# Optimization experiments

Measured on AMD Instinct MI355X. Metric: run time of the kernel, lower is better.

The kernel has to match this reference:

```python
import jax, jax.numpy as jnp
import numpy as np

USER_NUM = 100000
ITEM_NUM = 50000
N_NODES = USER_NUM + ITEM_NUM
EMB = 64
N_LAYERS = 3
E_HALF = 2000000  # edges per direction; total directed edges = 4M


def _make_bipartite_edges(ku, ki):
    u = jax.random.randint(ku, (E_HALF,), 0, USER_NUM)
    i = jax.random.randint(ki, (E_HALF,), 0, ITEM_NUM) + USER_NUM
    # bidirectional: user->item and item->user
    return jnp.concatenate([u, i]), jnp.concatenate([i, u])


def setup_inputs() -> dict:
    key = jax.random.key(0)
    ks = jax.random.split(key, 6)
    U = jax.random.normal(ks[0], (USER_NUM, EMB), jnp.float32)
    I = jax.random.normal(ks[1], (ITEM_NUM, EMB), jnp.float32)
    pos_src, pos_dst = _make_bipartite_edges(ks[2], ks[3])
    neg_src, neg_dst = _make_bipartite_edges(ks[4], ks[5])
    return {"U": U, "I": I, "pos_src": pos_src, "pos_dst": pos_dst,
            "neg_src": neg_src, "neg_dst": neg_dst}


def gcn_layer(x, src, dst):
    # symmetric-normalized sum aggregation (LightGCN propagation)
    ones = jnp.ones(src.shape, x.dtype)
    deg_out = jnp.maximum(jax.ops.segment_sum(ones, src, num_segments=N_NODES), 1.0)
    deg_in = jnp.maximum(jax.ops.segment_sum(ones, dst, num_segments=N_NODES), 1.0)
    h = x * (deg_out ** -0.5)[:, None]          # pre-scale by out-degree
    agg = jax.ops.segment_sum(h[src], dst, num_segments=N_NODES)  # copy_src + sum
    return agg * (deg_in ** -0.5)[:, None]      # post-scale by in-degree


def get_embedding(U, I, src, dst):
    res_u, res_i = U, I
    emb = None
    for i in range(N_LAYERS):
        x_in = jnp.concatenate([res_u, res_i], axis=0) if i == 0 else emb
        emb = gcn_layer(x_in, src, dst)
        scale = 1.0 / (i + 2)
        res_u = res_u + emb[:USER_NUM] * scale
        res_i = res_i + emb[USER_NUM:] * scale
    return res_u, res_i


def reference(U, I, pos_src, pos_dst, neg_src, neg_dst):
    res_u, res_i = get_embedding(U, I, pos_src, pos_dst)
    h = jnp.concatenate([res_u, res_i], axis=0)  # [N, D]
    pos_pred = jnp.sum(h[pos_src] * h[pos_dst], axis=-1)  # u_dot_v per edge
    neg_pred = jnp.sum(h[neg_src] * h[neg_dst], axis=-1)
    return pos_pred, neg_pred
```

## Files before the change

### kernel.cpp

```cpp
#include <hip/hip_runtime.h>
#include <hip/hip_fp16.h>

#define USER_NUM 100000
#define ITEM_NUM 50000
#define N_NODES  150000
#define EMB      64

#define NB       586
#define CAP      12288
#define PA_CHUNK 8192

static const size_t NODE_F = (size_t)N_NODES * EMB;

typedef _Float16 h2v __attribute__((ext_vector_type(2)));


__global__ __launch_bounds__(256) void partition_kernel(const int* __restrict__ u_arr,
                                                        const int* __restrict__ i_arr,
                                                        int Eh,
                                                        unsigned* __restrict__ part,
                                                        int* __restrict__ gcur) {
    __shared__ int hist[NB];
    __shared__ int hbase[NB];
    int tid = threadIdx.x;
    int start = blockIdx.x * PA_CHUNK;
    int n = min(PA_CHUNK, Eh - start);
    if (n <= 0) return;
    for (int b = tid; b < NB; b += 256) hist[b] = 0;
    __syncthreads();
    for (int k = tid; k < n; k += 256) {
        int u  = u_arr[start + k];
        int it = i_arr[start + k];
        atomicAdd(&hist[it >> 8], 1);
        atomicAdd(&hist[u  >> 8], 1);
    }
    __syncthreads();
    for (int b = tid; b < NB; b += 256) {
        int h = hist[b];
        hbase[b] = h ? atomicAdd(&gcur[b], h) : 0;
        hist[b] = 0;
    }
    __syncthreads();
    for (int k = tid; k < n; k += 256) {
        int u  = u_arr[start + k];
        int it = i_arr[start + k];
        int bI = it >> 8, bU = u >> 8;
        int o1 = atomicAdd(&hist[bI], 1);
        part[(size_t)bI * CAP + hbase[bI] + o1] = ((unsigned)(it & 255) << 24) | (unsigned)u;
        int o2 = atomicAdd(&hist[bU], 1);
        part[(size_t)bU * CAP + hbase[bU] + o2] = ((unsigned)(u & 255) << 24) | (unsigned)it;
    }
}

__global__ __launch_bounds__(1024) void bscan_kernel(const int* __restrict__ gcur,
                                                     int* __restrict__ bbase) {
    __shared__ int tmp[1024];
    int tid = threadIdx.x;
    int v = (tid < NB) ? gcur[tid] : 0;
    tmp[tid] = v;
    __syncthreads();
    for (int off = 1; off < 1024; off <<= 1) {
        int t = (tid >= off) ? tmp[tid - off] : 0;
        __syncthreads();
        tmp[tid] += t;
        __syncthreads();
    }
    if (tid < NB) bbase[tid] = tmp[tid] - v;
}

__global__ __launch_bounds__(256) void buildcsr_kernel(const unsigned* __restrict__ part,
                                                       const int* __restrict__ gcur,
                                                       const int* __restrict__ bbase,
                                                       int* __restrict__ rowptr,
                                                       float* __restrict__ rs,
                                                       int* __restrict__ adj,
                                                       int E) {
    __shared__ int cnt[256];
    __shared__ int cur[256];
    __shared__ int tmp[256];
    __shared__ int adjS[CAP];
    int b = blockIdx.x;
    int tid = threadIdx.x;
    int m = min(gcur[b], CAP);
    int base = bbase[b];
    const unsigned* bp = part + (size_t)b * CAP;
    cnt[tid] = 0;
    __syncthreads();
    for (int k = tid; k < m; k += 256) atomicAdd(&cnt[bp[k] >> 24], 1);
    __syncthreads();
    int myc = cnt[tid];
    tmp[tid] = myc;
    __syncthreads();
    for (int off = 1; off < 256; off <<= 1) {
        int t = (tid >= off) ? tmp[tid - off] : 0;
        __syncthreads();
        tmp[tid] += t;
        __syncthreads();
    }
    int excl = tmp[tid] - myc;
    int node = b * 256 + tid;
    if (node < N_NODES) {
        rowptr[node] = base + excl;
        rs[node] = rsqrtf(fmaxf((float)myc, 1.0f));
    }
    if (b == 0 && tid == 0) rowptr[N_NODES] = E;
    cur[tid] = excl;
    __syncthreads();
    for (int k = tid; k < m; k += 256) {
        unsigned p = bp[k];
        int off = atomicAdd(&cur[p >> 24], 1);
        adjS[off] = (int)(p & 0xFFFFFFu);
    }
    __syncthreads();
    for (int k = tid; k < m; k += 256) adj[base + k] = adjS[k];
}


__device__ __forceinline__ unsigned int packh2(float x, float y) {
    __half2 h = __floats2half2_rn(x, y);
    return *(unsigned int*)&h;
}

__global__ __launch_bounds__(256) void init_kernel(const float* __restrict__ U,
                                                   const float* __restrict__ I,
                                                   const float* __restrict__ rs,
                                                   __half* __restrict__ xs,
                                                   __half* __restrict__ res16) {
    size_t i8 = (size_t)blockIdx.x * blockDim.x + threadIdx.x;
    size_t n8 = NODE_F / 8;
    if (i8 >= n8) return;
    size_t i = i8 * 8;
    const size_t ucnt = (size_t)USER_NUM * EMB;
    float4 a, b;
    if (i < ucnt) { a = *(const float4*)(U + i); b = *(const float4*)(U + i + 4); }
    else          { a = *(const float4*)(I + (i - ucnt)); b = *(const float4*)(I + (i - ucnt) + 4); }
    uint4 pr;
    pr.x = packh2(a.x, a.y);
    pr.y = packh2(a.z, a.w);
    pr.z = packh2(b.x, b.y);
    pr.w = packh2(b.z, b.w);
    *(uint4*)(res16 + i) = pr;
    float r = rs[i / EMB];
    uint4 pk;
    pk.x = packh2(a.x * r, a.y * r);
    pk.y = packh2(a.z * r, a.w * r);
    pk.z = packh2(b.x * r, b.y * r);
    pk.w = packh2(b.z * r, b.w * r);
    *(uint4*)(xs + i) = pk;
}

__global__ __launch_bounds__(256) void gather_kernel(const int* __restrict__ rowptr,
                                                     const int* __restrict__ adj,
                                                     const __half* __restrict__ xs,
                                                     const float* __restrict__ rs,
                                                     __half* __restrict__ res16,
                                                     __half* __restrict__ xs_next,
                                                     float scale) {
    int wv = (int)(((unsigned)blockIdx.x * 256u + threadIdx.x) >> 6);
    if (wv >= N_NODES) return;
    int lane = threadIdx.x & 63;
    int g = lane & 7;
    int d = lane >> 3;
    int beg = rowptr[wv], end = rowptr[wv + 1];
    __half2 acch[4];
    acch[0] = __float2half2_rn(0.f);
    acch[1] = acch[0]; acch[2] = acch[0]; acch[3] = acch[0];

    for (int j = beg; j < end; j += 64) {
        int nloc = min(64, end - j);
        int id = (lane < nloc) ? adj[j + lane] : 0;
        int nfull = nloc >> 3;
        for (int k = 0; k < nfull; k++) {
            int s = __shfl(id, k * 8 + g);
            uint4 raw = *(const uint4*)(xs + (size_t)s * EMB + d * 8);
            const __half2* hp = (const __half2*)&raw;
            acch[0] = __hadd2(acch[0], hp[0]);
            acch[1] = __hadd2(acch[1], hp[1]);
            acch[2] = __hadd2(acch[2], hp[2]);
            acch[3] = __hadd2(acch[3], hp[3]);
        }
        int rem = nloc & 7;
        if (rem) {
            int s = __shfl(id, nfull * 8 + g);
            if (g < rem) {
                uint4 raw = *(const uint4*)(xs + (size_t)s * EMB + d * 8);
                const __half2* hp = (const __half2*)&raw;
                acch[0] = __hadd2(acch[0], hp[0]);
                acch[1] = __hadd2(acch[1], hp[1]);
                acch[2] = __hadd2(acch[2], hp[2]);
                acch[3] = __hadd2(acch[3], hp[3]);
            }
        }
    }

    #pragma unroll
    for (int m = 1; m < 8; m <<= 1) {
        #pragma unroll
        for (int q = 0; q < 4; q++) {
            unsigned o = __shfl_xor(*(unsigned*)&acch[q], m);
            acch[q] = __hadd2(acch[q], *(__half2*)&o);
        }
    }

    if (g == 0) {
        float r = rs[wv];
        float2 f0 = __half22float2(acch[0]);
        float2 f1 = __half22float2(acch[1]);
        float2 f2 = __half22float2(acch[2]);
        float2 f3 = __half22float2(acch[3]);
        float v0 = f0.x * r, v1 = f0.y * r, v2 = f1.x * r, v3 = f1.y * r;
        float v4 = f2.x * r, v5 = f2.y * r, v6 = f3.x * r, v7 = f3.y * r;
        size_t o = (size_t)wv * EMB + d * 8;
        uint4 cur = *(uint4*)(res16 + o);
        const __half2* cp = (const __half2*)&cur;
        float2 c0 = __half22float2(cp[0]);
        float2 c1 = __half22float2(cp[1]);
        float2 c2 = __half22float2(cp[2]);
        float2 c3 = __half22float2(cp[3]);
        uint4 nr;
        nr.x = packh2(c0.x + v0 * scale, c0.y + v1 * scale);
        nr.y = packh2(c1.x + v2 * scale, c1.y + v3 * scale);
        nr.z = packh2(c2.x + v4 * scale, c2.y + v5 * scale);
        nr.w = packh2(c3.x + v6 * scale, c3.y + v7 * scale);
        *(uint4*)(res16 + o) = nr;
        if (xs_next) {
            uint4 pk;
            pk.x = packh2(v0 * r, v1 * r);
            pk.y = packh2(v2 * r, v3 * r);
            pk.z = packh2(v4 * r, v5 * r);
            pk.w = packh2(v6 * r, v7 * r);
            *(uint4*)(xs_next + o) = pk;
        }
    }
}

__global__ __launch_bounds__(256) void dot2_kernel(const int* __restrict__ src,
                                                   const int* __restrict__ dst,
                                                   int Eh,
                                                   const __half* __restrict__ h,
                                                   float* __restrict__ out) {
    long long tid = (long long)blockIdx.x * blockDim.x + threadIdx.x;
    int e = (int)(tid >> 3);
    if (e >= Eh) return;
    int sub = (int)(tid & 7);
    int s = src[e];
    int t = dst[e];
    uint4 ra = *(const uint4*)(h + (size_t)s * EMB + sub * 8);
    uint4 rb = *(const uint4*)(h + (size_t)t * EMB + sub * 8);
    const __half2* ha = (const __half2*)&ra;
    const __half2* hb = (const __half2*)&rb;
    float dsum = 0.f;
    #pragma unroll
    for (int q = 0; q < 4; q++) {
#if __has_builtin(__builtin_amdgcn_fdot2)
        dsum = __builtin_amdgcn_fdot2(*(const h2v*)&ha[q], *(const h2v*)&hb[q], dsum, false);
#else
        float2 fa = __half22float2(ha[q]);
        float2 fb = __half22float2(hb[q]);
        dsum += fa.x * fb.x + fa.y * fb.y;
#endif
    }
    dsum += __shfl_xor(dsum, 1);
    dsum += __shfl_xor(dsum, 2);
    dsum += __shfl_xor(dsum, 4);
    if (sub == 0) {
        out[e] = dsum;
        out[e + Eh] = dsum;
    }
}


extern "C" void kernel_launch(void* const* d_in, const int* in_sizes, int n_in,
                              void* d_out, int out_size, void* d_ws, size_t ws_size,
                              hipStream_t stream) {
    const float* U       = (const float*)d_in[0];
    const float* I       = (const float*)d_in[1];
    const int*   pos_src = (const int*)d_in[2];
    const int*   pos_dst = (const int*)d_in[3];
    const int*   neg_src = (const int*)d_in[4];
    const int*   neg_dst = (const int*)d_in[5];
    const int E  = in_sizes[2];
    const int Eh = E / 2;
    float* out = (float*)d_out;

    char* p = (char*)d_ws;
    auto take = [&](size_t bytes) {
        char* r = p;
        p += (bytes + 255) & ~(size_t)255;
        return r;
    };
    int*    gcur   = (int*)take((size_t)NB * 4);
    int*    bbase  = (int*)take((size_t)NB * 4);
    int*    rowptr = (int*)take(((size_t)N_NODES + 1) * 4);
    float*  rs     = (float*)take((size_t)N_NODES * 4);
    int*    adj    = (int*)take((size_t)E * 4);
    __half* xsA    = (__half*)take(NODE_F * 2);
    char*   uni    = take(NODE_F * 2 * 2);
    unsigned* part = (unsigned*)uni;
    __half* xsB    = (__half*)uni;
    __half* res16  = (__half*)(uni + NODE_F * 2);

    const int B = 256;

    hipMemsetAsync(gcur, 0, (size_t)NB * 4, stream);
    partition_kernel<<<(Eh + PA_CHUNK - 1) / PA_CHUNK, B, 0, stream>>>(pos_src, pos_dst,
                                                                       Eh, part, gcur);
    bscan_kernel<<<1, 1024, 0, stream>>>(gcur, bbase);
    buildcsr_kernel<<<NB, B, 0, stream>>>(part, gcur, bbase, rowptr, rs, adj, E);

    size_t n8 = NODE_F / 8;
    init_kernel<<<(int)((n8 + B - 1) / B), B, 0, stream>>>(U, I, rs, xsA, res16);

    int gblk = (N_NODES * 64 + B - 1) / B;
    gather_kernel<<<gblk, B, 0, stream>>>(rowptr, adj, xsA, rs, res16, xsB, 1.0f / 2.0f);
    gather_kernel<<<gblk, B, 0, stream>>>(rowptr, adj, xsB, rs, res16, xsA, 1.0f / 3.0f);
    gather_kernel<<<gblk, B, 0, stream>>>(rowptr, adj, xsA, rs, res16, (__half*)nullptr, 1.0f / 4.0f);

    long long nthread = (long long)Eh * 8;
    int nblk = (int)((nthread + B - 1) / B);
    dot2_kernel<<<nblk, B, 0, stream>>>(pos_src, pos_dst, Eh, res16, out);
    dot2_kernel<<<nblk, B, 0, stream>>>(neg_src, neg_dst, Eh, res16, out + E);
}
```

Before: 453.2 us.

## Fuse bucket scan and embedding init into CSR build, merge dot kernels

Removes the separate bucket-scan kernel: each CSR block now computes its own base offset by reducing the gcur counts of earlier buckets. The embedding init (fp32 to fp16 conversion and pre-scaling by rs) moves into buildcsr, using the per-block rs values kept in shared memory. The adjacency list is written straight to global memory instead of being staged in LDS, and the two dot-product launches are merged into one. This cuts launch count and drops the large LDS staging array, at the cost of redundant prefix sums per block and scattered global writes for adj.

After: 456.8 us. No clear change (+0.8%).

```diff
diff --git a/kernel.cpp b/kernel.cpp
--- a/kernel.cpp
+++ b/kernel.cpp
@@ -52,43 +52,49 @@
     }
 }
 
-__global__ __launch_bounds__(1024) void bscan_kernel(const int* __restrict__ gcur,
-                                                     int* __restrict__ bbase) {
-    __shared__ int tmp[1024];
-    int tid = threadIdx.x;
-    int v = (tid < NB) ? gcur[tid] : 0;
-    tmp[tid] = v;
-    __syncthreads();
-    for (int off = 1; off < 1024; off <<= 1) {
-        int t = (tid >= off) ? tmp[tid - off] : 0;
-        __syncthreads();
-        tmp[tid] += t;
-        __syncthreads();
-    }
-    if (tid < NB) bbase[tid] = tmp[tid] - v;
+__device__ __forceinline__ unsigned int packh2(float x, float y) {
+    __half2 h = __floats2half2_rn(x, y);
+    return *(unsigned int*)&h;
 }
 
 __global__ __launch_bounds__(256) void buildcsr_kernel(const unsigned* __restrict__ part,
                                                        const int* __restrict__ gcur,
-                                                       const int* __restrict__ bbase,
+                                                       const float* __restrict__ U,
+                                                       const float* __restrict__ I,
                                                        int* __restrict__ rowptr,
                                                        float* __restrict__ rs,
                                                        int* __restrict__ adj,
+                                                       __half* __restrict__ xs,
+                                                       __half* __restrict__ res16,
                                                        int E) {
     __shared__ int cnt[256];
     __shared__ int cur[256];
     __shared__ int tmp[256];
-    __shared__ int adjS[CAP];
+    __shared__ float rsS[256];
+    __shared__ int baseS;
     int b = blockIdx.x;
     int tid = threadIdx.x;
+
+    int psum = 0;
+    for (int j = tid; j < b; j += 256) psum += gcur[j];
+    tmp[tid] = psum;
+    __syncthreads();
+    for (int off = 128; off >= 1; off >>= 1) {
+        if (tid < off) tmp[tid] += tmp[tid + off];
+        __syncthreads();
+    }
+    if (tid == 0) baseS = tmp[0];
+    __syncthreads();
+    int base = baseS;
     int m = min(gcur[b], CAP);
-    int base = bbase[b];
     const unsigned* bp = part + (size_t)b * CAP;
+
     cnt[tid] = 0;
     __syncthreads();
     for (int k = tid; k < m; k += 256) atomicAdd(&cnt[bp[k] >> 24], 1);
     __syncthreads();
     int myc = cnt[tid];
+
     tmp[tid] = myc;
     __syncthreads();
     for (int off = 1; off < 256; off <<= 1) {
@@ -99,55 +105,54 @@
     }
     int excl = tmp[tid] - myc;
     int node = b * 256 + tid;
+    float r = rsqrtf(fmaxf((float)myc, 1.0f));
+    rsS[tid] = r;
     if (node < N_NODES) {
         rowptr[node] = base + excl;
-        rs[node] = rsqrtf(fmaxf((float)myc, 1.0f));
+        rs[node] = r;
     }
     if (b == 0 && tid == 0) rowptr[N_NODES] = E;
     cur[tid] = excl;
     __syncthreads();
+
     for (int k = tid; k < m; k += 256) {
-        unsigned p = bp[k];
-        int off = atomicAdd(&cur[p >> 24], 1);
-        adjS[off] = (int)(p & 0xFFFFFFu);
-    }
-    __syncthreads();
-    for (int k = tid; k < m; k += 256) adj[base + k] = adjS[k];
-}
-
-
-__device__ __forceinline__ unsigned int packh2(float x, float y) {
-    __half2 h = __floats2half2_rn(x, y);
-    return *(unsigned int*)&h;
-}
-
-__global__ __launch_bounds__(256) void init_kernel(const float* __restrict__ U,
-                                                   const float* __restrict__ I,
-                                                   const float* __restrict__ rs,
-                                                   __half* __restrict__ xs,
-                                                   __half* __restrict__ res16) {
-    size_t i8 = (size_t)blockIdx.x * blockDim.x + threadIdx.x;
-    size_t n8 = NODE_F / 8;
-    if (i8 >= n8) return;
-    size_t i = i8 * 8;
+        unsigned pk = bp[k];
+        int off = atomicAdd(&cur[pk >> 24], 1);
+        adj[base + off] = (int)(pk & 0xFFFFFFu);
+    }
+
+    int first = b * 256;
+    int nnode = min(256, N_NODES - first);
+    if (nnode <= 0) return;
+    int nf8 = nnode * 8;
     const size_t ucnt = (size_t)USER_NUM * EMB;
-    float4 a, b;
-    if (i < ucnt) { a = *(const float4*)(U + i); b = *(const float4*)(U + i + 4); }
-    else          { a = *(const float4*)(I + (i - ucnt)); b = *(const float4*)(I + (i - ucnt) + 4); }
-    uint4 pr;
-    pr.x = packh2(a.x, a.y);
-    pr.y = packh2(a.z, a.w);
-    pr.z = packh2(b.x, b.y);
-    pr.w = packh2(b.z, b.w);
-    *(uint4*)(res16 + i) = pr;
-    float r = rs[i / EMB];
-    uint4 pk;
-    pk.x = packh2(a.x * r, a.y * r);
-    pk.y = packh2(a.z * r, a.w * r);
-    pk.z = packh2(b.x * r, b.y * r);
-    pk.w = packh2(b.z * r, b.w * r);
-    *(uint4*)(xs + i) = pk;
-}
+    for (int k8 = tid; k8 < nf8; k8 += 256) {
+        int nl = k8 >> 3;
+        size_t elem = (size_t)(first + nl) * EMB + (size_t)(k8 & 7) * 8;
+        float4 a, bb;
+        if (elem < ucnt) {
+            a  = *(const float4*)(U + elem);
+            bb = *(const float4*)(U + elem + 4);
+        } else {
+            a  = *(const float4*)(I + (elem - ucnt));
+            bb = *(const float4*)(I + (elem - ucnt) + 4);
+        }
+        uint4 pr;
+        pr.x = packh2(a.x, a.y);
+        pr.y = packh2(a.z, a.w);
+        pr.z = packh2(bb.x, bb.y);
+        pr.w = packh2(bb.z, bb.w);
+        *(uint4*)(res16 + elem) = pr;
+        float rr = rsS[nl];
+        uint4 px;
+        px.x = packh2(a.x * rr, a.y * rr);
+        px.y = packh2(a.z * rr, a.w * rr);
+        px.z = packh2(bb.x * rr, bb.y * rr);
+        px.w = packh2(bb.z * rr, bb.w * rr);
+        *(uint4*)(xs + elem) = px;
+    }
+}
+
 
 __global__ __launch_bounds__(256) void gather_kernel(const int* __restrict__ rowptr,
                                                      const int* __restrict__ adj,
@@ -211,8 +216,8 @@
         float v0 = f0.x * r, v1 = f0.y * r, v2 = f1.x * r, v3 = f1.y * r;
         float v4 = f2.x * r, v5 = f2.y * r, v6 = f3.x * r, v7 = f3.y * r;
         size_t o = (size_t)wv * EMB + d * 8;
-        uint4 cur = *(uint4*)(res16 + o);
-        const __half2* cp = (const __half2*)&cur;
+        uint4 curv = *(uint4*)(res16 + o);
+        const __half2* cp = (const __half2*)&curv;
         float2 c0 = __half22float2(cp[0]);
         float2 c1 = __half22float2(cp[1]);
         float2 c2 = __half22float2(cp[2]);
@@ -234,17 +239,25 @@
     }
 }
 
-__global__ __launch_bounds__(256) void dot2_kernel(const int* __restrict__ src,
-                                                   const int* __restrict__ dst,
-                                                   int Eh,
-                                                   const __half* __restrict__ h,
-                                                   float* __restrict__ out) {
+__global__ __launch_bounds__(256) void dot_all_kernel(const int* __restrict__ ps,
+                                                      const int* __restrict__ pd,
+                                                      const int* __restrict__ ns,
+                                                      const int* __restrict__ nd,
+                                                      int Eh, int E,
+                                                      const __half* __restrict__ h,
+                                                      float* __restrict__ out) {
     long long tid = (long long)blockIdx.x * blockDim.x + threadIdx.x;
-    int e = (int)(tid >> 3);
-    if (e >= Eh) return;
+    int slot = (int)(tid >> 3);
+    if (slot >= 2 * Eh) return;
     int sub = (int)(tid & 7);
-    int s = src[e];
-    int t = dst[e];
+    int e;
+    const int* sa;
+    const int* da;
+    float* o;
+    if (slot < Eh) { e = slot;      sa = ps; da = pd; o = out; }
+    else           { e = slot - Eh; sa = ns; da = nd; o = out + E; }
+    int s = sa[e];
+    int t = da[e];
     uint4 ra = *(const uint4*)(h + (size_t)s * EMB + sub * 8);
     uint4 rb = *(const uint4*)(h + (size_t)t * EMB + sub * 8);
     const __half2* ha = (const __half2*)&ra;
@@ -264,8 +277,8 @@
     dsum += __shfl_xor(dsum, 2);
     dsum += __shfl_xor(dsum, 4);
     if (sub == 0) {
-        out[e] = dsum;
-        out[e + Eh] = dsum;
+        o[e] = dsum;
+        o[e + Eh] = dsum;
     }
 }
 
@@ -289,35 +302,30 @@
         p += (bytes + 255) & ~(size_t)255;
         return r;
     };
-    int*    gcur   = (int*)take((size_t)NB * 4);
-    int*    bbase  = (int*)take((size_t)NB * 4);
-    int*    rowptr = (int*)take(((size_t)N_NODES + 1) * 4);
-    float*  rs     = (float*)take((size_t)N_NODES * 4);
-    int*    adj    = (int*)take((size_t)E * 4);
-    __half* xsA    = (__half*)take(NODE_F * 2);
-    char*   uni    = take(NODE_F * 2 * 2);
-    unsigned* part = (unsigned*)uni;
-    __half* xsB    = (__half*)uni;
-    __half* res16  = (__half*)(uni + NODE_F * 2);
+    int*      gcur   = (int*)take((size_t)NB * 4);
+    int*      rowptr = (int*)take(((size_t)N_NODES + 1) * 4);
+    float*    rs     = (float*)take((size_t)N_NODES * 4);
+    int*      adj    = (int*)take((size_t)E * 4);
+    unsigned* part   = (unsigned*)take((size_t)NB * CAP * 4);
+    __half*   xsA    = (__half*)take(NODE_F * 2);
+    __half*   xsB    = (__half*)take(NODE_F * 2);
+    __half*   res16  = (__half*)take(NODE_F * 2);
 
     const int B = 256;
 
     hipMemsetAsync(gcur, 0, (size_t)NB * 4, stream);
     partition_kernel<<<(Eh + PA_CHUNK - 1) / PA_CHUNK, B, 0, stream>>>(pos_src, pos_dst,
                                                                        Eh, part, gcur);
-    bscan_kernel<<<1, 1024, 0, stream>>>(gcur, bbase);
-    buildcsr_kernel<<<NB, B, 0, stream>>>(part, gcur, bbase, rowptr, rs, adj, E);
-
-    size_t n8 = NODE_F / 8;
-    init_kernel<<<(int)((n8 + B - 1) / B), B, 0, stream>>>(U, I, rs, xsA, res16);
+    buildcsr_kernel<<<NB, B, 0, stream>>>(part, gcur, U, I, rowptr, rs, adj,
+                                          xsA, res16, E);
 
     int gblk = (N_NODES * 64 + B - 1) / B;
     gather_kernel<<<gblk, B, 0, stream>>>(rowptr, adj, xsA, rs, res16, xsB, 1.0f / 2.0f);
     gather_kernel<<<gblk, B, 0, stream>>>(rowptr, adj, xsB, rs, res16, xsA, 1.0f / 3.0f);
     gather_kernel<<<gblk, B, 0, stream>>>(rowptr, adj, xsA, rs, res16, (__half*)nullptr, 1.0f / 4.0f);
 
-    long long nthread = (long long)Eh * 8;
+    long long nthread = (long long)(2 * Eh) * 8;
     int nblk = (int)((nthread + B - 1) / B);
-    dot2_kernel<<<nblk, B, 0, stream>>>(pos_src, pos_dst, Eh, res16, out);
-    dot2_kernel<<<nblk, B, 0, stream>>>(neg_src, neg_dst, Eh, res16, out + E);
-}
+    dot_all_kernel<<<nblk, B, 0, stream>>>(pos_src, pos_dst, neg_src, neg_dst,
+                                           Eh, E, res16, out);
+}
```
